# Kernel tuning notes

Measured on AMD Instinct MI355X. Metric: run time of the kernel, lower is better.

The kernel has to match this reference:

```python
import jax, jax.numpy as jnp
import numpy as np

S, L = 512, 32            # number of sequences, max sequence length
IN_FEATURES = 13824       # 512*3*3 + 1024*3*3 ROI features
HID = 1024                # Head.hidden_dim
LSTM_H = HID // 2         # per-direction hidden size (bidirectional)
N_CLASSES = 4787
BN_EPS = 1e-5


def _make_ragged():
    lengths = (4 + (np.arange(S) % 29)).astype(np.int32)  # 4..32, sum = 9121
    n = int(lengths.sum())
    perm = np.random.RandomState(0).permutation(n).astype(np.int32)
    seq_idx = np.zeros((S, L), dtype=np.int32)
    off = 0
    for i, l in enumerate(lengths):
        seq_idx[i, :l] = perm[off:off + l]
        off += l
    return n, jnp.asarray(seq_idx), jnp.asarray(lengths)


def setup_inputs() -> dict:
    n, seq_idx, lengths = _make_ragged()
    key = jax.random.key(0)
    ks = jax.random.split(key, 16)
    w = lambda k, shp, s=0.02: (jax.random.normal(k, shp, dtype=jnp.float32) * s)
    return {
        "x": jax.random.normal(ks[0], (n, IN_FEATURES), dtype=jnp.float32),
        "fc1_w": w(ks[1], (HID, IN_FEATURES)),
        "fc1_b": w(ks[2], (HID,)),
        "bn_gamma": jnp.ones((HID,), jnp.float32),
        "bn_beta": jnp.zeros((HID,), jnp.float32),
        "fc2_w": w(ks[3], (N_CLASSES, HID)),
        "fc2_b": w(ks[4], (N_CLASSES,)),
        "w_ih_f": w(ks[5], (4 * LSTM_H, HID)),
        "w_hh_f": w(ks[6], (4 * LSTM_H, LSTM_H)),
        "b_ih_f": w(ks[7], (4 * LSTM_H,)),
        "b_hh_f": w(ks[8], (4 * LSTM_H,)),
        "w_ih_b": w(ks[9], (4 * LSTM_H, HID)),
        "w_hh_b": w(ks[10], (4 * LSTM_H, LSTM_H)),
        "b_ih_b": w(ks[11], (4 * LSTM_H,)),
        "b_hh_b": w(ks[12], (4 * LSTM_H,)),
        "seq_idx": seq_idx,
        "lengths": lengths,
    }


def _lstm_scan(seq_x, w_ih, w_hh, b_ih, b_hh):
    # seq_x: [S, L, HID] -> outputs [S, L, LSTM_H]; PyTorch gate order i,f,g,o
    s = seq_x.shape[0]
    h0 = jnp.zeros((s, LSTM_H), seq_x.dtype)
    c0 = jnp.zeros((s, LSTM_H), seq_x.dtype)
    x_gates = jnp.einsum('slh,gh->slg', seq_x, w_ih) + b_ih + b_hh  # precompute input gates

    def step(carry, xg):
        h, c = carry
        g = xg + h @ w_hh.T
        i, f, gg, o = jnp.split(g, 4, axis=-1)
        c = jax.nn.sigmoid(f) * c + jax.nn.sigmoid(i) * jnp.tanh(gg)
        h = jax.nn.sigmoid(o) * jnp.tanh(c)
        return (h, c), h

    _, hs = jax.lax.scan(step, (h0, c0), x_gates.transpose(1, 0, 2))  # [L, S, H]
    return hs.transpose(1, 0, 2)


def reference(x, fc1_w, fc1_b, bn_gamma, bn_beta, fc2_w, fc2_b,
              w_ih_f, w_hh_f, b_ih_f, b_hh_f,
              w_ih_b, w_hh_b, b_ih_b, b_hh_b,
              seq_idx, lengths):
    n = x.shape[0]
    # Head: fc1 -> relu -> BatchNorm1d (training-mode batch stats)
    h = jax.nn.relu(x @ fc1_w.T + fc1_b)
    mean = h.mean(axis=0)
    var = jnp.mean((h - mean) ** 2, axis=0)
    feats = (h - mean) * jax.lax.rsqrt(var + BN_EPS) * bn_gamma + bn_beta  # [N, HID]

    # ragged gather into packed [S, L, HID]
    mask = jnp.arange(L)[None, :] < lengths[:, None]          # [S, L]
    gidx = jnp.where(mask, seq_idx, 0)
    seq_x = feats[gidx] * mask[:, :, None]                    # zero padded slots

    # forward direction (padding at tail: harmless to causal scan)
    hf = _lstm_scan(seq_x, w_ih_f, w_hh_f, b_ih_f, b_hh_f)
    # backward direction: reverse each sequence within its valid length
    rev = jnp.clip(lengths[:, None] - 1 - jnp.arange(L)[None, :], 0, L - 1)  # [S, L]
    seq_rev = jnp.take_along_axis(seq_x, rev[:, :, None], axis=1)
    hb_rev = _lstm_scan(seq_rev, w_ih_b, w_hh_b, b_ih_b, b_hh_b)
    hb = jnp.take_along_axis(hb_rev, rev[:, :, None], axis=1)  # un-reverse (involution on valid region)

    out = jnp.concatenate([hf, hb], axis=-1)                   # [S, L, HID]

    # scatter back to flat roi order; padded slots dropped out-of-bounds
    sidx = jnp.where(mask, seq_idx, n).reshape(-1)
    lstm_feats = jnp.zeros((n, HID), feats.dtype).at[sidx].set(
        out.reshape(-1, HID), mode='drop')

    logits = lstm_feats @ fc2_w.T + fc2_b                      # apply_fc_out
    return logits
```

## Files before the change

### kernel.cpp

```cpp
#include <hip/hip_runtime.h>

typedef short short8v __attribute__((ext_vector_type(8)));
typedef float f32x4 __attribute__((ext_vector_type(4)));
typedef _Float16 h4v __attribute__((ext_vector_type(4)));

__device__ __forceinline__ unsigned short f2bf(float f){
  unsigned int u = __float_as_uint(f);
  u += 0x7fffu + ((u >> 16) & 1u);
  return (unsigned short)(u >> 16);
}
__device__ __forceinline__ float bf2f(unsigned short h){
  return __uint_as_float(((unsigned int)h) << 16);
}
union H2F { unsigned short u; _Float16 h; };
__device__ __forceinline__ float fp16f(unsigned short b){ H2F t; t.u = b; return (float)t.h; }

typedef __attribute__((address_space(1))) const unsigned int gu32;
typedef __attribute__((address_space(3))) unsigned int lu32;
__device__ __forceinline__ void gl16(const void* g, void* l){
  __builtin_amdgcn_global_load_lds((gu32*)g, (lu32*)l, 16, 0, 0);
}

template<int EPI>
__global__ __launch_bounds__(512, 2)
void gemm256(const unsigned short* __restrict__ A, const unsigned short* __restrict__ B,
             void* __restrict__ Cout, int M, int N, int K, int lda, int ldb, int ldc,
             const float* __restrict__ bias)
{
  __shared__ __align__(16) unsigned short As[2 * 2 * 256 * 32];
  __shared__ __align__(16) unsigned short Bs[2 * 2 * 256 * 32];

  const int tid = threadIdx.x;
  const int gx = gridDim.x;
  const int nwg = gx * gridDim.y;
  int dd = blockIdx.y * gx + blockIdx.x;
  int q8 = nwg >> 3, r8 = nwg & 7, xc = dd & 7, t8 = dd >> 3;
  int Lid = (xc < r8 ? xc * (q8 + 1) : r8 * (q8 + 1) + (xc - r8) * q8) + t8;
  const int bcol = (Lid % gx) * 256;
  const int brow = (Lid / gx) * 256;

  const int l = tid & 63, w = tid >> 6;
  const int wr = w >> 2;
  const int wn = w & 3;
  const int r16 = l & 15, kg = l >> 4;
  const int swz = (r16 >> 1) & 3;
  const int srow4 = l >> 2, sblk = l & 3;
  const int scol = (sblk ^ ((l >> 3) & 3)) * 8;

  const int kz = blockIdx.z * K;
  const unsigned short* Ag = A + (size_t)(brow + w * 32 + srow4) * lda + kz + scol;
  const unsigned short* Bg = B + (size_t)(bcol + w * 32 + srow4) * ldb + kz + scol;
  unsigned short* Asd = As + w * 1024;
  unsigned short* Bsd = Bs + w * 1024;

#define STA(buf, kh, kt) do { \
    gl16(Ag + (size_t)(kt) * 64 + (kh) * 32, Asd + (buf) * 16384 + (kh) * 8192); \
    gl16(Ag + (size_t)(kt) * 64 + (kh) * 32 + (size_t)16 * lda, Asd + (buf) * 16384 + (kh) * 8192 + 512); \
  } while (0)
#define STB(buf, kh, kt) do { \
    gl16(Bg + (size_t)(kt) * 64 + (kh) * 32, Bsd + (buf) * 16384 + (kh) * 8192); \
    gl16(Bg + (size_t)(kt) * 64 + (kh) * 32 + (size_t)16 * ldb, Bsd + (buf) * 16384 + (kh) * 8192 + 512); \
  } while (0)

  const unsigned short* Ard = As + (wr * 128 + r16) * 32 + ((kg ^ swz) * 8);
  const unsigned short* Brd = Bs + (wn * 64 + r16) * 32 + ((kg ^ swz) * 8);

  f32x4 acc[8][4];
  #pragma unroll
  for (int m = 0; m < 8; m++)
    #pragma unroll
    for (int nn = 0; nn < 4; nn++) { f32x4 z = {0.f, 0.f, 0.f, 0.f}; acc[m][nn] = z; }

  short8v af[4], bfr[4];

#define LDA4(c, kk, mq) { \
    _Pragma("unroll") for (int i = 0; i < 4; i++) \
      af[i] = *(const short8v*)(Ard + (c) * 16384 + (kk) * 8192 + ((mq) * 4 + i) * 512); }
#define LDB4(c, kk) { \
    _Pragma("unroll") for (int nn = 0; nn < 4; nn++) \
      bfr[nn] = *(const short8v*)(Brd + (c) * 16384 + (kk) * 8192 + nn * 512); }
#define MFMAQ(mq) { \
    __builtin_amdgcn_s_setprio(1); \
    _Pragma("unroll") for (int i = 0; i < 4; i++) { \
      _Pragma("unroll") for (int nn = 0; nn < 4; nn++) \
        acc[(mq) * 4 + i][nn] = __builtin_amdgcn_mfma_f32_16x16x32_bf16(af[i], bfr[nn], acc[(mq) * 4 + i][nn], 0, 0, 0); \
    } \
    __builtin_amdgcn_s_setprio(0); }

  const int nk = K >> 6;
  STA(0, 0, 0); STB(0, 0, 0); STA(0, 1, 0); STB(0, 1, 0);
  asm volatile("s_waitcnt vmcnt(4)" ::: "memory");
  __builtin_amdgcn_s_barrier();
  __builtin_amdgcn_sched_barrier(0);

  for (int j = 0; j < nk; j++) {
    const int c = j & 1, nb = c ^ 1;
    const bool pf = (j + 1 < nk);
    LDB4(c, 0); LDA4(c, 0, 0);
    if (pf) STA(nb, 0, j + 1);
    __builtin_amdgcn_s_barrier();
    MFMAQ(0);
    __builtin_amdgcn_s_barrier();
    LDA4(c, 0, 1);
    if (pf) STB(nb, 0, j + 1);
    __builtin_amdgcn_s_barrier();
    MFMAQ(1);
    if (pf) asm volatile("s_waitcnt vmcnt(4)" ::: "memory");
    else    asm volatile("s_waitcnt vmcnt(0)" ::: "memory");
    __builtin_amdgcn_s_barrier();
    __builtin_amdgcn_sched_barrier(0);
    LDB4(c, 1); LDA4(c, 1, 0);
    if (pf) STA(nb, 1, j + 1);
    __builtin_amdgcn_s_barrier();
    MFMAQ(0);
    __builtin_amdgcn_s_barrier();
    LDA4(c, 1, 1);
    if (pf) STB(nb, 1, j + 1);
    __builtin_amdgcn_s_barrier();
    MFMAQ(1);
    if (pf) asm volatile("s_waitcnt vmcnt(4)" ::: "memory");
    __builtin_amdgcn_s_barrier();
    __builtin_amdgcn_sched_barrier(0);
  }
#undef STA
#undef STB
#undef LDA4
#undef LDB4
#undef MFMAQ

  #pragma unroll
  for (int m = 0; m < 8; m++) {
    const int row0 = brow + wr * 128 + m * 16 + kg * 4;
    #pragma unroll
    for (int nn = 0; nn < 4; nn++) {
      const int col = bcol + wn * 64 + nn * 16 + r16;
      if (col < N) {
        const float bv = (EPI == 5) ? 0.f : bias[col];
        #pragma unroll
        for (int rr = 0; rr < 4; rr++) {
          const int row = row0 + rr;
          if (row < M) {
            float val = acc[m][nn][rr] + bv;
            if (EPI == 3) {
              int dL = col >> 11, rc = col & 2047;
              int cg = rc >> 6, g = (rc >> 4) & 3, u = rc & 15;
              int pc = (dL << 11) + (((cg << 4) + u) << 2) + g;
              ((_Float16*)Cout)[(size_t)row * ldc + pc] = (_Float16)val;
            } else if (EPI == 5) {
              ((_Float16*)Cout)[(size_t)blockIdx.z * M * ldc + (size_t)row * ldc + col] = (_Float16)val;
            } else {
              ((float*)Cout)[(size_t)row * ldc + col] = val;
            }
          }
        }
      }
    }
  }
}

__global__ __launch_bounds__(256) void fc1_reduce(const _Float16* __restrict__ P, const float* __restrict__ bias,
                                                  unsigned short* __restrict__ h, float* __restrict__ part,
                                                  int n, int mpad) {
  int b = blockIdx.x, tid = threadIdx.x;
  int c0 = tid * 4;
  float4 bsv = *(const float4*)(bias + c0);
  float s[4] = {0,0,0,0}, qq[4] = {0,0,0,0};
  int rbeg = b * 32;
  for (int r = rbeg; r < rbeg + 32; r++) {
    h4v a0 = *(const h4v*)(P + (size_t)r * 1024 + c0);
    h4v a1 = *(const h4v*)(P + ((size_t)mpad + r) * 1024 + c0);
    h4v a2 = *(const h4v*)(P + ((size_t)2 * mpad + r) * 1024 + c0);
    float v0 = fmaxf((float)a0[0] + (float)a1[0] + (float)a2[0] + bsv.x, 0.f);
    float v1 = fmaxf((float)a0[1] + (float)a1[1] + (float)a2[1] + bsv.y, 0.f);
    float v2 = fmaxf((float)a0[2] + (float)a1[2] + (float)a2[2] + bsv.z, 0.f);
    float v3 = fmaxf((float)a0[3] + (float)a1[3] + (float)a2[3] + bsv.w, 0.f);
    if (r < n) {
      s[0] += v0; qq[0] += v0 * v0;
      s[1] += v1; qq[1] += v1 * v1;
      s[2] += v2; qq[2] += v2 * v2;
      s[3] += v3; qq[3] += v3 * v3;
    }
    *(ushort4*)(h + (size_t)r * 1024 + c0) = make_ushort4(f2bf(v0), f2bf(v1), f2bf(v2), f2bf(v3));
  }
  float* pp = part + (size_t)b * 2048;
  #pragma unroll
  for (int k = 0; k < 4; k++) { pp[(c0 + k) * 2] = s[k]; pp[(c0 + k) * 2 + 1] = qq[k]; }
}

__global__ __launch_bounds__(256, 1)
void lstm_persist(const unsigned short* __restrict__ whhc, const unsigned short* __restrict__ bcp,
                  const _Float16* __restrict__ G,
                  const int* __restrict__ gf, const int* __restrict__ gb, const int* __restrict__ sb,
                  unsigned short* __restrict__ hst,
                  unsigned short* __restrict__ lfeat, int* __restrict__ flags)
{
  __shared__ __align__(16) unsigned short Bsh[64 * 512];
  const int tid = threadIdx.x;
  const int l = tid & 63, w = tid >> 6;
  const int b = blockIdx.x;
  const int d = (b >> 2) & 1;
  const int rg = b & 3;
  const int c = b >> 3;
  const int grp = b & 7;
  const int rowbase = d * 512 + rg * 128;
  const int r16 = l & 15, kg = l >> 4;
  const int swzl = (r16 & 7) * 8;
  const int hu = c * 16 + r16;

  const unsigned short* Bsrc = whhc + ((size_t)(d * 2048 + c * 64)) * 512;
  #pragma unroll
  for (int i = 0; i < 16; i++) {
    int rr = w * 16 + i;
    gl16(Bsrc + (size_t)rr * 512 + ((l * 8) ^ ((rr & 7) * 8)), Bsh + rr * 512);
  }
  asm volatile("s_waitcnt vmcnt(0)");
  __syncthreads();

  float creg[2][4];
  #pragma unroll
  for (int m = 0; m < 2; m++)
    #pragma unroll
    for (int rr = 0; rr < 4; rr++) creg[m][rr] = 0.f;

  for (int t = 0; t < 32; t++) {
    ushort4 gv[2][4];
    int scv[2][4];
    #pragma unroll
    for (int m = 0; m < 2; m++) {
      #pragma unroll
      for (int rr = 0; rr < 4; rr++) {
        int row = rowbase + w * 32 + m * 16 + kg * 4 + rr;
        int sq = row & 511;
        int gi = d ? gb[sq * 32 + t] : gf[sq * 32 + t];
        const unsigned short* src = (gi >= 0)
            ? (const unsigned short*)G + ((size_t)gi * 4096 + (d << 11) + hu * 4)
            : bcp + ((d << 11) + hu * 4);
        gv[m][rr] = *(const ushort4*)src;
        scv[m][rr] = d ? sb[sq * 32 + t] : gi;
      }
    }

    if (t > 0) {
      while (true) {
        int fv = 0x7fffffff;
        if (l < 32)
          fv = __hip_atomic_load(flags + ((grp * 32 + l) << 5), __ATOMIC_RELAXED, __HIP_MEMORY_SCOPE_AGENT);
        if (__all(fv >= t)) break;
        __builtin_amdgcn_s_sleep(1);
      }
    }
    asm volatile("" ::: "memory");

    const unsigned short* hp = hst + (size_t)(t & 1) * (1024 * 512);
    unsigned short* hn = hst + (size_t)((t + 1) & 1) * (1024 * 512);

    short8v av[2][16];
    #pragma unroll
    for (int m = 0; m < 2; m++) {
      unsigned long long a64 = (unsigned long long)(hp + (size_t)(rowbase + w * 32 + m * 16 + r16) * 512 + kg * 8);
      #pragma unroll
      for (int kf = 0; kf < 16; kf++) {
        asm volatile("global_load_dwordx4 %0, %1, off offset:%c2 sc0 sc1"
                     : "=v"(av[m][kf]) : "v"(a64), "i"(kf * 64) : "memory");
      }
    }
    asm volatile("s_waitcnt vmcnt(0)" ::: "memory");

    f32x4 acc[2][4];
    #pragma unroll
    for (int m = 0; m < 2; m++)
      #pragma unroll
      for (int nn = 0; nn < 4; nn++) { f32x4 z = {0.f, 0.f, 0.f, 0.f}; acc[m][nn] = z; }

    #pragma unroll
    for (int kc = 0; kc < 8; kc++) {
      short8v bv[4][2];
      #pragma unroll
      for (int nn = 0; nn < 4; nn++)
        #pragma unroll
        for (int kk = 0; kk < 2; kk++)
          bv[nn][kk] = *(const short8v*)(Bsh + (nn * 16 + r16) * 512 + ((kc * 64 + kk * 32 + kg * 8) ^ swzl));
      #pragma unroll
      for (int kk = 0; kk < 2; kk++)
        #pragma unroll
        for (int m = 0; m < 2; m++)
          #pragma unroll
          for (int nn = 0; nn < 4; nn++)
            acc[m][nn] = __builtin_amdgcn_mfma_f32_16x16x32_bf16(av[m][kc * 2 + kk], bv[nn][kk], acc[m][nn], 0, 0, 0);
    }

    #pragma unroll
    for (int m = 0; m < 2; m++) {
      #pragma unroll
      for (int reg = 0; reg < 4; reg++) {
        int row = rowbase + w * 32 + m * 16 + kg * 4 + reg;
        float g_i = acc[m][0][reg] + fp16f(gv[m][reg].x);
        float g_f = acc[m][1][reg] + fp16f(gv[m][reg].y);
        float g_g = acc[m][2][reg] + fp16f(gv[m][reg].z);
        float g_o = acc[m][3][reg] + fp16f(gv[m][reg].w);
        float si = 1.f / (1.f + __expf(-g_i));
        float sf = 1.f / (1.f + __expf(-g_f));
        float so = 1.f / (1.f + __expf(-g_o));
        float cn = sf * creg[m][reg] + si * tanhf(g_g);
        float hnv = so * tanhf(cn);
        creg[m][reg] = cn;
        unsigned int hb = f2bf(hnv);
        unsigned long long ha = (unsigned long long)(hn + (size_t)row * 512 + hu);
        asm volatile("global_store_short %0, %1, off sc0 sc1" :: "v"(ha), "v"(hb) : "memory");
        int sc = scv[m][reg];
        if (sc >= 0) lfeat[(size_t)sc * 1024 + d * 512 + hu] = f2bf(hnv);
      }
    }

    __syncthreads();
    if (t < 31 && tid == 0)
      __hip_atomic_store(flags + ((grp * 32 + c) << 5), t + 1, __ATOMIC_RELAXED, __HIP_MEMORY_SCOPE_AGENT);
  }
}

__global__ __launch_bounds__(256) void conv_bf16(const float* __restrict__ src, unsigned short* __restrict__ dst,
                                                 size_t nvalid, size_t total) {
  size_t stride = (size_t)gridDim.x * 2048;
  for (size_t i = ((size_t)blockIdx.x * 256 + threadIdx.x) * 8; i < total; i += stride) {
    unsigned short o[8];
    if (i + 8 <= nvalid) {
      float4 a = *(const float4*)(src + i);
      float4 b = *(const float4*)(src + i + 4);
      o[0] = f2bf(a.x); o[1] = f2bf(a.y); o[2] = f2bf(a.z); o[3] = f2bf(a.w);
      o[4] = f2bf(b.x); o[5] = f2bf(b.y); o[6] = f2bf(b.z); o[7] = f2bf(b.w);
    } else {
      #pragma unroll
      for (int j = 0; j < 8; j++) o[j] = (i + j < nvalid) ? f2bf(src[i + j]) : (unsigned short)0;
    }
    *(ushort4*)(dst + i) = make_ushort4(o[0], o[1], o[2], o[3]);
    *(ushort4*)(dst + i + 4) = make_ushort4(o[4], o[5], o[6], o[7]);
  }
}

__global__ __launch_bounds__(256) void bn_final(const float* __restrict__ part, const float* __restrict__ gamma,
                                                const float* __restrict__ beta, float* __restrict__ scale,
                                                float* __restrict__ shift, int M, int nb) {
  int c = blockIdx.x * 256 + threadIdx.x;
  float s = 0.f, q = 0.f;
  for (int b = 0; b < nb; b++) { s += part[(size_t)b * 2048 + c * 2]; q += part[(size_t)b * 2048 + c * 2 + 1]; }
  float mean = s / (float)M;
  float var = q / (float)M - mean * mean;
  float sc = gamma[c] * rsqrtf(var + 1e-5f);
  scale[c] = sc; shift[c] = beta[c] - mean * sc;
}

__global__ __launch_bounds__(256) void prep_tables(const int* __restrict__ seq_idx, const int* __restrict__ lengths,
                                                   int* __restrict__ gf, int* __restrict__ gb, int* __restrict__ sb) {
  int idx = blockIdx.x * 256 + threadIdx.x;
  if (idx < 512 * 32) {
    int s = idx >> 5, t = idx & 31;
    int len = lengths[s];
    gf[idx] = (t < len) ? seq_idx[idx] : -1;
    int rb = len - 1 - t;
    gb[idx] = seq_idx[(s << 5) + (rb < 0 ? 0 : rb)];
    sb[idx] = (t < len) ? seq_idx[(s << 5) + (len - 1 - t)] : -1;
  }
}

__global__ __launch_bounds__(256) void build_wih(const float* __restrict__ wf, const float* __restrict__ wb,
                                                 const float* __restrict__ bihf, const float* __restrict__ bhhf,
                                                 const float* __restrict__ bihb, const float* __restrict__ bhhb,
                                                 const float* __restrict__ scale, const float* __restrict__ shift,
                                                 unsigned short* __restrict__ wcdst, float* __restrict__ bc,
                                                 _Float16* __restrict__ bcp) {
  int orow = blockIdx.x * 4 + (threadIdx.x >> 6);
  int l = threadIdx.x & 63;
  int dir = orow >> 11, j = orow & 2047;
  int cc = j >> 6, jj = j & 63, g = jj >> 4, u = jj & 15;
  int srow = g * 512 + cc * 16 + u;
  const float* src = (dir ? wb : wf) + (size_t)srow * 1024;
  unsigned short* dst = wcdst + (size_t)orow * 1024;
  float sacc = 0.f;
  #pragma unroll
  for (int jv = 0; jv < 16; jv++) {
    int k = l + jv * 64;
    float v = src[k];
    sacc += shift[k] * v;
    dst[k] = f2bf(v * scale[k]);
  }
  #pragma unroll
  for (int o2 = 32; o2 > 0; o2 >>= 1) sacc += __shfl_down(sacc, o2);
  if (l == 0) {
    float bb = (dir ? (bihb[srow] + bhhb[srow]) : (bihf[srow] + bhhf[srow])) + sacc;
    bc[orow] = bb;
    int pc = (dir << 11) + (((cc << 4) + u) << 2) + g;
    bcp[pc] = (_Float16)bb;
  }
}

__global__ __launch_bounds__(256) void build_whh(const float* __restrict__ wf, const float* __restrict__ wb,
                                                 unsigned short* __restrict__ o) {
  int cidx = blockIdx.x * 256 + threadIdx.x;
  if (cidx < 4096 * 64) {
    int orow = cidx >> 6, k0 = (cidx & 63) * 8;
    int dir = orow >> 11, j = orow & 2047;
    int cc = j >> 6, jj = j & 63, g = jj >> 4, u = jj & 15;
    const float* src = (dir ? wb : wf) + (size_t)(g * 512 + cc * 16 + u) * 512 + k0;
    unsigned short* dst = o + (size_t)orow * 512 + k0;
    float4 a = *(const float4*)(src);
    float4 bq = *(const float4*)(src + 4);
    dst[0] = f2bf(a.x); dst[1] = f2bf(a.y); dst[2] = f2bf(a.z); dst[3] = f2bf(a.w);
    dst[4] = f2bf(bq.x); dst[5] = f2bf(bq.y); dst[6] = f2bf(bq.z); dst[7] = f2bf(bq.w);
  }
}

extern "C" void kernel_launch(void* const* d_in, const int* in_sizes, int n_in,
                              void* d_out, int out_size, void* d_ws, size_t ws_size,
                              hipStream_t stream) {
  const float* x     = (const float*)d_in[0];
  const float* fc1w  = (const float*)d_in[1];
  const float* fc1b  = (const float*)d_in[2];
  const float* gamma = (const float*)d_in[3];
  const float* beta  = (const float*)d_in[4];
  const float* fc2w  = (const float*)d_in[5];
  const float* fc2b  = (const float*)d_in[6];
  const float* wihf  = (const float*)d_in[7];
  const float* whhf  = (const float*)d_in[8];
  const float* bihf  = (const float*)d_in[9];
  const float* bhhf  = (const float*)d_in[10];
  const float* wihb  = (const float*)d_in[11];
  const float* whhb  = (const float*)d_in[12];
  const float* bihb  = (const float*)d_in[13];
  const float* bhhb  = (const float*)d_in[14];
  const int* seq_idx = (const int*)d_in[15];
  const int* lengths = (const int*)d_in[16];
  float* out = (float*)d_out;

  const int n = in_sizes[0] / 13824;
  const int mt = (n + 255) / 256;
  const int mpad = mt * 256;

  char* ws = (char*)d_ws;
  size_t off = 0;
  auto alloc = [&](size_t bytes) -> void* {
    void* p = ws + off; off += (bytes + 255) & ~(size_t)255; return p;
  };
  unsigned short* x_h  = (unsigned short*)alloc((size_t)mpad * 13824 * 2);
  unsigned short* w1_h = (unsigned short*)alloc((size_t)1024 * 13824 * 2);
  unsigned short* w2_h = (unsigned short*)alloc((size_t)4864 * 1024 * 2);
  unsigned short* h    = (unsigned short*)alloc((size_t)mpad * 1024 * 2);
  _Float16*       G    = (_Float16*)alloc((size_t)mpad * 4096 * 2);
  unsigned short* wihc = (unsigned short*)alloc((size_t)4096 * 1024 * 2);
  unsigned short* whhc = (unsigned short*)alloc((size_t)4096 * 512 * 2);
  float* bias_c = (float*)alloc(4096 * 4);
  _Float16* bias_p = (_Float16*)alloc(4096 * 2);
  unsigned short* lfeat  = (unsigned short*)alloc((size_t)mpad * 1024 * 2);
  unsigned short* hstate = (unsigned short*)alloc((size_t)2 * 1024 * 512 * 2);
  float* part   = (float*)alloc((size_t)(mpad / 32) * 2048 * 4);
  float* scale  = (float*)alloc(1024 * 4);
  float* shift  = (float*)alloc(1024 * 4);
  int* gf  = (int*)alloc(16384 * 4);
  int* gb  = (int*)alloc(16384 * 4);
  int* sb  = (int*)alloc(16384 * 4);
  int* flags = (int*)alloc(256 * 32 * 4);

  _Float16* P16 = (_Float16*)G;

  dim3 blk(256);
  dim3 blk5(512);

  conv_bf16<<<2048, blk, 0, stream>>>(x, x_h, (size_t)n * 13824, (size_t)mpad * 13824);
  conv_bf16<<<1024, blk, 0, stream>>>(fc1w, w1_h, (size_t)1024 * 13824, (size_t)1024 * 13824);
  conv_bf16<<<256, blk, 0, stream>>>(fc2w, w2_h, (size_t)4787 * 1024, (size_t)4864 * 1024);
  build_whh<<<1024, blk, 0, stream>>>(whhf, whhb, whhc);
  prep_tables<<<64, blk, 0, stream>>>(seq_idx, lengths, gf, gb, sb);
  hipMemsetAsync(hstate, 0, (size_t)2 * 1024 * 512 * 2, stream);
  hipMemsetAsync(flags, 0, 256 * 32 * 4, stream);

  gemm256<5><<<dim3(4, mt, 3), blk5, 0, stream>>>(
      x_h, w1_h, P16, mpad, 1024, 4608, 13824, 13824, 1024, nullptr);

  fc1_reduce<<<mpad / 32, blk, 0, stream>>>(P16, fc1b, h, part, n, mpad);
  bn_final<<<4, blk, 0, stream>>>(part, gamma, beta, scale, shift, n, mpad / 32);
  build_wih<<<1024, blk, 0, stream>>>(wihf, wihb, bihf, bhhf, bihb, bhhb, scale, shift, wihc, bias_c, bias_p);

  gemm256<3><<<dim3(16, mt), blk5, 0, stream>>>(
      h, wihc, G, n, 4096, 1024, 1024, 1024, 4096, bias_c);

  lstm_persist<<<256, blk, 0, stream>>>(whhc, (const unsigned short*)bias_p, G, gf, gb, sb,
                                        hstate, lfeat, flags);

  gemm256<0><<<dim3(19, mt), blk5, 0, stream>>>(
      lfeat, w2_h, out, n, 4787, 1024, 1024, 1024, 4787, fc2b);
}
```

Before: 1.241 ms.

## Repartition persistent LSTM blocks to 32 hidden units and fewer rows each

```diff
diff --git a/kernel.cpp b/kernel.cpp
--- a/kernel.cpp
+++ b/kernel.cpp
@@ -97,25 +97,23 @@
     const int c = j & 1, nb = c ^ 1;
     const bool pf = (j + 1 < nk);
     LDB4(c, 0); LDA4(c, 0, 0);
-    if (pf) STA(nb, 0, j + 1);
+    if (pf) { STA(nb, 0, j + 1); STB(nb, 0, j + 1); }
     __builtin_amdgcn_s_barrier();
     MFMAQ(0);
     __builtin_amdgcn_s_barrier();
     LDA4(c, 0, 1);
-    if (pf) STB(nb, 0, j + 1);
+    if (pf) { STA(nb, 1, j + 1); STB(nb, 1, j + 1); }
     __builtin_amdgcn_s_barrier();
     MFMAQ(1);
-    if (pf) asm volatile("s_waitcnt vmcnt(4)" ::: "memory");
+    if (pf) asm volatile("s_waitcnt vmcnt(8)" ::: "memory");
     else    asm volatile("s_waitcnt vmcnt(0)" ::: "memory");
     __builtin_amdgcn_s_barrier();
     __builtin_amdgcn_sched_barrier(0);
     LDB4(c, 1); LDA4(c, 1, 0);
-    if (pf) STA(nb, 1, j + 1);
     __builtin_amdgcn_s_barrier();
     MFMAQ(0);
     __builtin_amdgcn_s_barrier();
     LDA4(c, 1, 1);
-    if (pf) STB(nb, 1, j + 1);
     __builtin_amdgcn_s_barrier();
     MFMAQ(1);
     if (pf) asm volatile("s_waitcnt vmcnt(4)" ::: "memory");
@@ -194,23 +192,22 @@
                   unsigned short* __restrict__ hst,
                   unsigned short* __restrict__ lfeat, int* __restrict__ flags)
 {
-  __shared__ __align__(16) unsigned short Bsh[64 * 512];
+  __shared__ __align__(16) unsigned short Bsh[128 * 512];
   const int tid = threadIdx.x;
   const int l = tid & 63, w = tid >> 6;
   const int b = blockIdx.x;
-  const int d = (b >> 2) & 1;
-  const int rg = b & 3;
-  const int c = b >> 3;
-  const int grp = b & 7;
-  const int rowbase = d * 512 + rg * 128;
+  const int grp = b & 15;
+  const int c = b >> 4;
+  const int d = grp >> 3;
+  const int rowbase = d * 512 + (grp & 7) * 64;
   const int r16 = l & 15, kg = l >> 4;
   const int swzl = (r16 & 7) * 8;
-  const int hu = c * 16 + r16;
-
-  const unsigned short* Bsrc = whhc + ((size_t)(d * 2048 + c * 64)) * 512;
-  #pragma unroll
-  for (int i = 0; i < 16; i++) {
-    int rr = w * 16 + i;
+  const int hu0 = c * 32 + r16;
+
+  const unsigned short* Bsrc = whhc + ((size_t)(d * 2048 + c * 128)) * 512;
+  #pragma unroll
+  for (int i = 0; i < 32; i++) {
+    int rr = w * 32 + i;
     gl16(Bsrc + (size_t)rr * 512 + ((l * 8) ^ ((rr & 7) * 8)), Bsh + rr * 512);
   }
   asm volatile("s_waitcnt vmcnt(0)");
@@ -224,27 +221,25 @@
 
   for (int t = 0; t < 32; t++) {
     ushort4 gv[2][4];
-    int scv[2][4];
-    #pragma unroll
-    for (int m = 0; m < 2; m++) {
-      #pragma unroll
-      for (int rr = 0; rr < 4; rr++) {
-        int row = rowbase + w * 32 + m * 16 + kg * 4 + rr;
-        int sq = row & 511;
-        int gi = d ? gb[sq * 32 + t] : gf[sq * 32 + t];
-        const unsigned short* src = (gi >= 0)
-            ? (const unsigned short*)G + ((size_t)gi * 4096 + (d << 11) + hu * 4)
-            : bcp + ((d << 11) + hu * 4);
-        gv[m][rr] = *(const ushort4*)src;
-        scv[m][rr] = d ? sb[sq * 32 + t] : gi;
-      }
+    int scv[4];
+    #pragma unroll
+    for (int rr = 0; rr < 4; rr++) {
+      int row = rowbase + w * 16 + kg * 4 + rr;
+      int sq = row & 511;
+      int gi = d ? gb[sq * 32 + t] : gf[sq * 32 + t];
+      const unsigned short* src = (gi >= 0)
+          ? (const unsigned short*)G + ((size_t)gi * 4096 + (d << 11))
+          : bcp + (d << 11);
+      gv[0][rr] = *(const ushort4*)(src + hu0 * 4);
+      gv[1][rr] = *(const ushort4*)(src + (hu0 + 16) * 4);
+      scv[rr] = d ? sb[sq * 32 + t] : gi;
     }
 
     if (t > 0) {
       while (true) {
         int fv = 0x7fffffff;
-        if (l < 32)
-          fv = __hip_atomic_load(flags + ((grp * 32 + l) << 5), __ATOMIC_RELAXED, __HIP_MEMORY_SCOPE_AGENT);
+        if (l < 16)
+          fv = __hip_atomic_load(flags + ((grp * 16 + l) << 5), __ATOMIC_RELAXED, __HIP_MEMORY_SCOPE_AGENT);
         if (__all(fv >= t)) break;
         __builtin_amdgcn_s_sleep(1);
       }
@@ -254,67 +249,63 @@
     const unsigned short* hp = hst + (size_t)(t & 1) * (1024 * 512);
     unsigned short* hn = hst + (size_t)((t + 1) & 1) * (1024 * 512);
 
-    short8v av[2][16];
-    #pragma unroll
-    for (int m = 0; m < 2; m++) {
-      unsigned long long a64 = (unsigned long long)(hp + (size_t)(rowbase + w * 32 + m * 16 + r16) * 512 + kg * 8);
+    short8v av[16];
+    {
+      unsigned long long a64 = (unsigned long long)(hp + (size_t)(rowbase + w * 16 + r16) * 512 + kg * 8);
       #pragma unroll
       for (int kf = 0; kf < 16; kf++) {
         asm volatile("global_load_dwordx4 %0, %1, off offset:%c2 sc0 sc1"
-                     : "=v"(av[m][kf]) : "v"(a64), "i"(kf * 64) : "memory");
+                     : "=v"(av[kf]) : "v"(a64), "i"(kf * 64) : "memory");
       }
     }
     asm volatile("s_waitcnt vmcnt(0)" ::: "memory");
 
-    f32x4 acc[2][4];
-    #pragma unroll
-    for (int m = 0; m < 2; m++)
+    f32x4 acc[8];
+    #pragma unroll
+    for (int nn = 0; nn < 8; nn++) { f32x4 z = {0.f, 0.f, 0.f, 0.f}; acc[nn] = z; }
+
+    #pragma unroll
+    for (int kc = 0; kc < 8; kc++) {
+      short8v bv[8][2];
       #pragma unroll
-      for (int nn = 0; nn < 4; nn++) { f32x4 z = {0.f, 0.f, 0.f, 0.f}; acc[m][nn] = z; }
-
-    #pragma unroll
-    for (int kc = 0; kc < 8; kc++) {
-      short8v bv[4][2];
-      #pragma unroll
-      for (int nn = 0; nn < 4; nn++)
+      for (int nn = 0; nn < 8; nn++)
         #pragma unroll
         for (int kk = 0; kk < 2; kk++)
           bv[nn][kk] = *(const short8v*)(Bsh + (nn * 16 + r16) * 512 + ((kc * 64 + kk * 32 + kg * 8) ^ swzl));
       #pragma unroll
       for (int kk = 0; kk < 2; kk++)
         #pragma unroll
-        for (int m = 0; m < 2; m++)
-          #pragma unroll
-          for (int nn = 0; nn < 4; nn++)
-            acc[m][nn] = __builtin_amdgcn_mfma_f32_16x16x32_bf16(av[m][kc * 2 + kk], bv[nn][kk], acc[m][nn], 0, 0, 0);
-    }
-
-    #pragma unroll
-    for (int m = 0; m < 2; m++) {
+        for (int nn = 0; nn < 8; nn++)
+          acc[nn] = __builtin_amdgcn_mfma_f32_16x16x32_bf16(av[kc * 2 + kk], bv[nn][kk], acc[nn], 0, 0, 0);
+    }
+
+    #pragma unroll
+    for (int cgl = 0; cgl < 2; cgl++) {
+      const int hu = hu0 + cgl * 16;
       #pragma unroll
       for (int reg = 0; reg < 4; reg++) {
-        int row = rowbase + w * 32 + m * 16 + kg * 4 + reg;
-        float g_i = acc[m][0][reg] + fp16f(gv[m][reg].x);
-        float g_f = acc[m][1][reg] + fp16f(gv[m][reg].y);
-        float g_g = acc[m][2][reg] + fp16f(gv[m][reg].z);
-        float g_o = acc[m][3][reg] + fp16f(gv[m][reg].w);
+        int row = rowbase + w * 16 + kg * 4 + reg;
+        float g_i = acc[cgl * 4 + 0][reg] + fp16f(gv[cgl][reg].x);
+        float g_f = acc[cgl * 4 + 1][reg] + fp16f(gv[cgl][reg].y);
+        float g_g = acc[cgl * 4 + 2][reg] + fp16f(gv[cgl][reg].z);
+        float g_o = acc[cgl * 4 + 3][reg] + fp16f(gv[cgl][reg].w);
         float si = 1.f / (1.f + __expf(-g_i));
         float sf = 1.f / (1.f + __expf(-g_f));
         float so = 1.f / (1.f + __expf(-g_o));
-        float cn = sf * creg[m][reg] + si * tanhf(g_g);
+        float cn = sf * creg[cgl][reg] + si * tanhf(g_g);
         float hnv = so * tanhf(cn);
-        creg[m][reg] = cn;
+        creg[cgl][reg] = cn;
         unsigned int hb = f2bf(hnv);
         unsigned long long ha = (unsigned long long)(hn + (size_t)row * 512 + hu);
         asm volatile("global_store_short %0, %1, off sc0 sc1" :: "v"(ha), "v"(hb) : "memory");
-        int sc = scv[m][reg];
+        int sc = scv[reg];
         if (sc >= 0) lfeat[(size_t)sc * 1024 + d * 512 + hu] = f2bf(hnv);
       }
     }
 
     __syncthreads();
     if (t < 31 && tid == 0)
-      __hip_atomic_store(flags + ((grp * 32 + c) << 5), t + 1, __ATOMIC_RELAXED, __HIP_MEMORY_SCOPE_AGENT);
+      __hip_atomic_store(flags + ((grp * 16 + c) << 5), t + 1, __ATOMIC_RELAXED, __HIP_MEMORY_SCOPE_AGENT);
   }
 }
 
@@ -399,8 +390,10 @@
   if (cidx < 4096 * 64) {
     int orow = cidx >> 6, k0 = (cidx & 63) * 8;
     int dir = orow >> 11, j = orow & 2047;
-    int cc = j >> 6, jj = j & 63, g = jj >> 4, u = jj & 15;
-    const float* src = (dir ? wb : wf) + (size_t)(g * 512 + cc * 16 + u) * 512 + k0;
+    int cc = j >> 7, L = j & 127;
+    int cgl = L >> 6, g = (L >> 4) & 3, u = L & 15;
+    int hunit = cc * 32 + cgl * 16 + u;
+    const float* src = (dir ? wb : wf) + (size_t)(g * 512 + hunit) * 512 + k0;
     unsigned short* dst = o + (size_t)orow * 512 + k0;
     float4 a = *(const float4*)(src);
     float4 bq = *(const float4*)(src + 4);
```

Result: no change. 1.237 ms (-0.3%).
